# Kernel tuning notes

Hardware: AMD Instinct MI355X
Metric: run time of the kernel (lower is better)

## Reference

```python
import jax, jax.numpy as jnp
import numpy as np

HIDDEN = 128
SIGMA_D = 0.2
SIGMA_A = 15.0
ANGLE_K = 10
FACTOR_A = 180.0 / (SIGMA_A * np.pi)


def _div_term():
    half = HIDDEN // 2
    return jnp.exp(jnp.arange(half, dtype=jnp.float32) * (-np.log(10000.0) / half))


def _sinusoid(x):
    # x: float tensor of (integer-valued) indices; returns x.shape + (HIDDEN,)
    pos = x[..., None].astype(jnp.float32)
    dt = _div_term()
    s = jnp.sin(pos * dt)
    c = jnp.cos(pos * dt)
    # interleave: even channels sin, odd channels cos
    return jnp.stack([s, c], axis=-1).reshape(x.shape + (HIDDEN,))


def setup_inputs() -> dict:
    key = jax.random.key(0)
    k1, k2, k3, k4, k5 = jax.random.split(key, 5)
    B, N = 2, 1024
    scale = 1.0 / np.sqrt(HIDDEN)
    points = jax.random.normal(k1, (B, N, 3), dtype=jnp.float32)
    Wd = jax.random.normal(k2, (HIDDEN, HIDDEN), dtype=jnp.float32) * scale
    bd = jax.random.normal(k3, (HIDDEN,), dtype=jnp.float32) * scale
    Wa = jax.random.normal(k4, (HIDDEN, HIDDEN), dtype=jnp.float32) * scale
    ba = jax.random.normal(k5, (HIDDEN,), dtype=jnp.float32) * scale
    return {"points": points, "Wd": Wd, "bd": bd, "Wa": Wa, "ba": ba}


def _single(pts, Wd, bd, Wa, ba):
    # pts: (N, 3)
    n = pts.shape[0]
    diff = pts[:, None, :] - pts[None, :, :]            # (N, N, 3)
    dists = jnp.sqrt(jnp.sum(diff * diff, axis=-1))      # (N, N)
    idx_d = jnp.clip(jnp.round(dists / SIGMA_D), 0.0, 255.0)
    # k nearest neighbours (smallest distances, incl. self)
    _, nn = jax.lax.top_k(-dists, ANGLE_K)               # (N, K)
    vec = pts[nn] - pts[:, None, :]                      # (N, K, 3)
    vnorm = jnp.linalg.norm(vec, axis=-1, keepdims=True)
    unit = vec / (vnorm + 1e-8)
    cos_ang = jnp.clip(jnp.einsum('nkd,nld->nkl', unit, unit), -1.0, 1.0)
    angles = jnp.arccos(cos_ang)                         # (N, K, K)
    idx_a = jnp.clip(jnp.round(angles * FACTOR_A), 0.0, 255.0)
    # indices computed under no_grad in the original
    idx_d = jax.lax.stop_gradient(idx_d)
    idx_a = jax.lax.stop_gradient(idx_a)

    embed_d = _sinusoid(idx_d)                           # (N, N, C)
    embed_d = jnp.mean(embed_d @ Wd.T + bd, axis=1)      # (N, C)

    embed_a = _sinusoid(idx_a)                           # (N, K, K, C)
    embed_a = embed_a @ Wa.T + ba
    embed_a = jnp.max(embed_a.reshape(n, -1, HIDDEN), axis=1)  # (N, C)
    return embed_d + embed_a


def reference(points, Wd, bd, Wa, ba):
    return jax.vmap(_single, in_axes=(0, None, None, None, None))(points, Wd, bd, Wa, ba)
```

## Files before the change

kernel.cpp:

```cpp
#include <hip/hip_runtime.h>
#include <hip/hip_bf16.h>

#define NPTS 1024
#define HID 128
#define KNN 10
#define PPB 4
#define FLT_MAX_ 3.402823466e+38f

__global__ __launch_bounds__(512) void gse_build(
    const float* __restrict__ Wd, const float* __restrict__ bd,
    const float* __restrict__ Wa, const float* __restrict__ ba,
    const float* __restrict__ pts, int nP,
    float* __restrict__ Td, float* __restrict__ Ta, float4* __restrict__ P4) {
    const int blk = blockIdx.x;
    const int tid = threadIdx.x;

    if (tid < 8) {
        for (int idx = blk * 8 + tid; idx < nP; idx += 272 * 8) {
            P4[idx] = make_float4(pts[idx * 3 + 0], pts[idx * 3 + 1],
                                  pts[idx * 3 + 2], 0.0f);
        }
    }

    __shared__ float S[HID];
    __shared__ float part[512];
    const bool isA = (blk >= 256);
    const int v = isA ? blk - 256 : blk;
    const int c = tid & 127;
    const int seg = tid >> 7;

    if (tid < HID) {
        const int m = tid >> 1;
        const float dtm = expf((float)m * (float)(-9.210340371976184 / 64.0));
        const float arg = (float)v * dtm;
        S[tid] = (tid & 1) ? cosf(arg) : sinf(arg);
    }
    __syncthreads();

    const float* W = isA ? Wa : Wd;
    const float* wrow = W + c * HID + seg * 32;
    const float* srow = S + seg * 32;
    float acc = 0.0f;
    #pragma unroll
    for (int h = 0; h < 32; h += 4) {
        const float4 wv = *reinterpret_cast<const float4*>(wrow + h);
        acc += srow[h] * wv.x + srow[h + 1] * wv.y + srow[h + 2] * wv.z + srow[h + 3] * wv.w;
    }
    part[tid] = acc;
    __syncthreads();

    if (tid < HID) {
        const float s = (part[c] + part[c + 128]) + (part[c + 256] + part[c + 384]);
        if (isA) Ta[v * HID + c] = s + ba[c];
        else     Td[v * HID + c] = (s + bd[c]) * (1.0f / (float)NPTS);
    }
}

__global__ __launch_bounds__(1024, 8) void gse_main4(
    const float4* __restrict__ P4,
    const float* __restrict__ Td,
    const float* __restrict__ Ta,
    float* __restrict__ out) {
    const int tid = threadIdx.x;
    const int pt  = tid >> 8;
    const int t   = tid & 255;
    const int lane = tid & 63;
    const int w   = (tid >> 6) & 3;
    const int gid = blockIdx.x * PPB + pt;

    const int b = gid >> 10;
    const int i = gid & 1023;
    const float4* P = P4 + (size_t)b * NPTS;

    __shared__ int h4[PPB][4][256];
    __shared__ unsigned long long cand[PPB][64];
    __shared__ int nn[PPB][KNN];
    __shared__ float sums[PPB][256], mxs[PPB][256];
    __shared__ unsigned amask_s[PPB];
    __shared__ int ccnt[PPB];
    __shared__ int meta_s[PPB];

    {
        int* hf = (int*)h4[pt];
        hf[t] = 0; hf[t + 256] = 0; hf[t + 512] = 0; hf[t + 768] = 0;
    }
    if (t == 0) { amask_s[pt] = 0u; ccnt[pt] = 0; }
    const float4 p = P[i];
    __syncthreads();

    float d4[4];
    int q4[4];
    const int jb = w * 256;
    #pragma unroll
    for (int s = 0; s < 4; ++s) {
        const int j = jb + s * 64 + lane;
        const float4 q = P[j];
        const float dx = p.x - q.x;
        const float dy = p.y - q.y;
        const float dz = p.z - q.z;
        const float dd = sqrtf(dx * dx + dy * dy + dz * dz);
        d4[s] = dd;
        float qq = rintf(dd / 0.2f);
        qq = fminf(fmaxf(qq, 0.0f), 255.0f);
        q4[s] = (int)qq;
        atomicAdd(&h4[pt][w][q4[s]], 1);
    }
    __syncthreads();

    const int hsum = h4[pt][0][t] + h4[pt][1][t] + h4[pt][2][t] + h4[pt][3][t];
    h4[pt][0][t] = hsum;
    __syncthreads();
    const int* hist = h4[pt][0];

    if (w == 0) {
        int cum = hist[lane];
        #pragma unroll
        for (int off = 1; off < 64; off <<= 1) {
            const int n_ = __shfl_up(cum, off);
            if (lane >= off) cum += n_;
        }
        const unsigned long long bal = __ballot(cum >= KNN);
        const unsigned long long nz0 = __ballot(hist[lane] != 0);
        const unsigned long long nz1 = __ballot(hist[64 + lane] != 0);
        const unsigned long long nz2 = __ballot(hist[128 + lane] != 0);
        const unsigned long long nz3 = __ballot(hist[192 + lane] != 0);
        int maxbin;
        if (nz3)      maxbin = 192 + 63 - __clzll((long long)nz3);
        else if (nz2) maxbin = 128 + 63 - __clzll((long long)nz2);
        else if (nz1) maxbin = 64 + 63 - __clzll((long long)nz1);
        else          maxbin = 63 - __clzll((long long)nz0);
        int b10 = 0, c = 0;
        if (bal) { b10 = __ffsll(bal) - 1; c = __shfl(cum, b10); }
        const int fast = (bal != 0ull && c <= 64) ? 1 : 0;
        if (lane == 0) {
            meta_s[pt] = (b10 & 0xff) | ((fast ? c : 0) << 8)
                       | ((maxbin & 0xff) << 16) | (fast << 30);
        }
    }
    __syncthreads();
    const int meta = meta_s[pt];
    const int b10 = meta & 0xff;
    const int c = (meta >> 8) & 0xff;
    const int maxbin = (meta >> 16) & 0xff;
    const bool fast = ((meta >> 30) & 1) != 0;

    if (fast) {
        #pragma unroll
        for (int s = 0; s < 4; ++s) {
            const bool pred = (q4[s] <= b10);
            const unsigned long long m = __ballot(pred);
            if (m) {
                int base = 0;
                if (lane == 0) base = atomicAdd(&ccnt[pt], __popcll(m));
                base = __shfl(base, 0);
                if (pred) {
                    const int pos = base + (int)__popcll(m & ((1ull << lane) - 1ull));
                    const int idx = jb + s * 64 + lane;
                    cand[pt][pos] = ((unsigned long long)__float_as_uint(d4[s]) << 32)
                                  | (unsigned)idx;
                }
            }
        }
        __syncthreads();
        if (t < c) {
            const unsigned long long my = cand[pt][t];
            int rank = 0;
            #pragma unroll 8
            for (int pp = 0; pp < c; ++pp) {
                rank += (cand[pt][pp] < my) ? 1 : 0;
            }
            if (rank < KNN) nn[pt][rank] = (int)(my & 0xffffffffu);
        }
        __syncthreads();
    } else {
        unsigned valid = 0xfu;
        unsigned long long keep = 0;
        for (int r = 0; r < KNN; ++r) {
            float bv = FLT_MAX_;
            int bi = 0x7fffffff;
            #pragma unroll
            for (int s = 0; s < 4; ++s) {
                if (valid & (1u << s)) {
                    const float v_ = d4[s];
                    const int id_ = jb + s * 64 + lane;
                    if (v_ < bv || (v_ == bv && id_ < bi)) { bv = v_; bi = id_; }
                }
            }
            #pragma unroll
            for (int off = 32; off > 0; off >>= 1) {
                const float ov = __shfl_xor(bv, off);
                const int oi = __shfl_xor(bi, off);
                if (ov < bv || (ov == bv && oi < bi)) { bv = ov; bi = oi; }
            }
            const int loc = bi - jb;
            if (loc >= 0 && loc < 256 && lane == (loc & 63)) valid &= ~(1u << (loc >> 6));
            if (lane == r) keep = ((unsigned long long)__float_as_uint(bv) << 32)
                                | (unsigned)bi;
        }
        if (lane < KNN) cand[pt][w * KNN + lane] = keep;
        __syncthreads();
        if (t < 4 * KNN) {
            const unsigned long long my = cand[pt][t];
            int rank = 0;
            for (int pp = 0; pp < 4 * KNN; ++pp) {
                rank += (cand[pt][pp] < my) ? 1 : 0;
            }
            if (rank < KNN) nn[pt][rank] = (int)(my & 0xffffffffu);
        }
        __syncthreads();
    }

    if (t < KNN * KNN) {
        const int k = t / KNN, l = t % KNN;
        const int jk = nn[pt][k], jl = nn[pt][l];
        const float4 qk = P[jk];
        const float4 ql = P[jl];
        const float kx = qk.x - p.x;
        const float ky = qk.y - p.y;
        const float kz = qk.z - p.z;
        const float dk = sqrtf(kx * kx + ky * ky + kz * kz) + 1e-8f;
        const float lx = ql.x - p.x;
        const float ly = ql.y - p.y;
        const float lz = ql.z - p.z;
        const float dl = sqrtf(lx * lx + ly * ly + lz * lz) + 1e-8f;
        float cc = (kx / dk) * (lx / dl) + (ky / dk) * (ly / dl) + (kz / dk) * (lz / dl);
        cc = fminf(fmaxf(cc, -1.0f), 1.0f);
        const float ang = acosf(cc);
        float q = rintf(ang * (float)(180.0 / (15.0 * M_PI)));
        q = fminf(fmaxf(q, 0.0f), 15.0f);
        atomicOr(&amask_s[pt], 1u << (int)q);
    }
    __syncthreads();

    const unsigned am = amask_s[pt];
    const int c7 = t & 127;
    const int half = t >> 7;
    float s = 0.0f;
    const float* tdc = Td + c7;
    #pragma unroll 4
    for (int v = half; v <= maxbin; v += 2) {
        s += (float)hist[v] * tdc[v * HID];
    }
    float mx = -FLT_MAX_;
    const float* tac = Ta + c7;
    #pragma unroll
    for (int v = 0; v < 8; ++v) {
        const int vv = half * 8 + v;
        const float tv = tac[vv * HID];
        if (am & (1u << vv)) mx = fmaxf(mx, tv);
    }
    sums[pt][t] = s;
    mxs[pt][t] = mx;
    __syncthreads();
    if (t < HID) {
        out[(size_t)gid * HID + t] =
            (sums[pt][t] + sums[pt][t + 128]) + fmaxf(mxs[pt][t], mxs[pt][t + 128]);
    }
}

__global__ __launch_bounds__(256, 8) void gse_main(
    const float4* __restrict__ P4,
    const float* __restrict__ Td,
    const float* __restrict__ Ta,
    float* __restrict__ out) {
    const int gid = blockIdx.x;
    const int b = gid >> 10;
    const int i = gid & 1023;
    const float4* P = P4 + (size_t)b * NPTS;
    const int tid = threadIdx.x;
    const int lane = tid & 63;
    const int w = tid >> 6;

    __shared__ int h4[4][256];
    __shared__ unsigned long long cand[64];
    __shared__ int nn[KNN];
    __shared__ float sums[256], mxs[256];
    __shared__ unsigned amask_s;
    __shared__ int ccnt;
    __shared__ int meta_s;

    {
        int* hf = (int*)h4;
        hf[tid] = 0; hf[tid + 256] = 0; hf[tid + 512] = 0; hf[tid + 768] = 0;
    }
    if (tid == 0) { amask_s = 0u; ccnt = 0; }
    const float4 p = P[i];
    __syncthreads();

    float d4[4];
    int q4[4];
    const int jb = w * 256;
    #pragma unroll
    for (int s = 0; s < 4; ++s) {
        const int j = jb + s * 64 + lane;
        const float4 q = P[j];
        const float dx = p.x - q.x;
        const float dy = p.y - q.y;
        const float dz = p.z - q.z;
        const float dd = sqrtf(dx * dx + dy * dy + dz * dz);
        d4[s] = dd;
        float qq = rintf(dd / 0.2f);
        qq = fminf(fmaxf(qq, 0.0f), 255.0f);
        q4[s] = (int)qq;
        atomicAdd(&h4[w][q4[s]], 1);
    }
    __syncthreads();

    const int hsum = h4[0][tid] + h4[1][tid] + h4[2][tid] + h4[3][tid];
    h4[0][tid] = hsum;
    __syncthreads();
    const int* hist = h4[0];

    if (w == 0) {
        int cum = hist[lane];
        #pragma unroll
        for (int off = 1; off < 64; off <<= 1) {
            const int n_ = __shfl_up(cum, off);
            if (lane >= off) cum += n_;
        }
        const unsigned long long bal = __ballot(cum >= KNN);
        const unsigned long long nz0 = __ballot(hist[lane] != 0);
        const unsigned long long nz1 = __ballot(hist[64 + lane] != 0);
        const unsigned long long nz2 = __ballot(hist[128 + lane] != 0);
        const unsigned long long nz3 = __ballot(hist[192 + lane] != 0);
        int maxbin;
        if (nz3)      maxbin = 192 + 63 - __clzll((long long)nz3);
        else if (nz2) maxbin = 128 + 63 - __clzll((long long)nz2);
        else if (nz1) maxbin = 64 + 63 - __clzll((long long)nz1);
        else          maxbin = 63 - __clzll((long long)nz0);
        int b10 = 0, c = 0;
        if (bal) { b10 = __ffsll(bal) - 1; c = __shfl(cum, b10); }
        const int fast = (bal != 0ull && c <= 64) ? 1 : 0;
        if (lane == 0) {
            meta_s = (b10 & 0xff) | ((fast ? c : 0) << 8)
                   | ((maxbin & 0xff) << 16) | (fast << 30);
        }
    }
    __syncthreads();
    const int meta = meta_s;
    const int b10 = meta & 0xff;
    const int c = (meta >> 8) & 0xff;
    const int maxbin = (meta >> 16) & 0xff;
    const bool fast = ((meta >> 30) & 1) != 0;

    if (fast) {
        #pragma unroll
        for (int s = 0; s < 4; ++s) {
            const bool pred = (q4[s] <= b10);
            const unsigned long long m = __ballot(pred);
            if (m) {
                int base = 0;
                if (lane == 0) base = atomicAdd(&ccnt, __popcll(m));
                base = __shfl(base, 0);
                if (pred) {
                    const int pos = base + (int)__popcll(m & ((1ull << lane) - 1ull));
                    const int idx = jb + s * 64 + lane;
                    cand[pos] = ((unsigned long long)__float_as_uint(d4[s]) << 32)
                              | (unsigned)idx;
                }
            }
        }
        __syncthreads();
        if (tid < c) {
            const unsigned long long my = cand[tid];
            int rank = 0;
            #pragma unroll 8
            for (int pp = 0; pp < c; ++pp) rank += (cand[pp] < my) ? 1 : 0;
            if (rank < KNN) nn[rank] = (int)(my & 0xffffffffu);
        }
        __syncthreads();
    } else {
        unsigned valid = 0xfu;
        unsigned long long keep = 0;
        for (int r = 0; r < KNN; ++r) {
            float bv = FLT_MAX_;
            int bi = 0x7fffffff;
            #pragma unroll
            for (int s = 0; s < 4; ++s) {
                if (valid & (1u << s)) {
                    const float v_ = d4[s];
                    const int id_ = jb + s * 64 + lane;
                    if (v_ < bv || (v_ == bv && id_ < bi)) { bv = v_; bi = id_; }
                }
            }
            #pragma unroll
            for (int off = 32; off > 0; off >>= 1) {
                const float ov = __shfl_xor(bv, off);
                const int oi = __shfl_xor(bi, off);
                if (ov < bv || (ov == bv && oi < bi)) { bv = ov; bi = oi; }
            }
            const int loc = bi - jb;
            if (loc >= 0 && loc < 256 && lane == (loc & 63)) valid &= ~(1u << (loc >> 6));
            if (lane == r) keep = ((unsigned long long)__float_as_uint(bv) << 32)
                                | (unsigned)bi;
        }
        if (lane < KNN) cand[w * KNN + lane] = keep;
        __syncthreads();
        if (tid < 4 * KNN) {
            const unsigned long long my = cand[tid];
            int rank = 0;
            for (int pp = 0; pp < 4 * KNN; ++pp) rank += (cand[pp] < my) ? 1 : 0;
            if (rank < KNN) nn[rank] = (int)(my & 0xffffffffu);
        }
        __syncthreads();
    }

    if (tid < KNN * KNN) {
        const int k = tid / KNN, l = tid % KNN;
        const int jk = nn[k], jl = nn[l];
        const float4 qk = P[jk];
        const float4 ql = P[jl];
        const float kx = qk.x - p.x;
        const float ky = qk.y - p.y;
        const float kz = qk.z - p.z;
        const float dk = sqrtf(kx * kx + ky * ky + kz * kz) + 1e-8f;
        const float lx = ql.x - p.x;
        const float ly = ql.y - p.y;
        const float lz = ql.z - p.z;
        const float dl = sqrtf(lx * lx + ly * ly + lz * lz) + 1e-8f;
        float cc = (kx / dk) * (lx / dl) + (ky / dk) * (ly / dl) + (kz / dk) * (lz / dl);
        cc = fminf(fmaxf(cc, -1.0f), 1.0f);
        const float ang = acosf(cc);
        float q = rintf(ang * (float)(180.0 / (15.0 * M_PI)));
        q = fminf(fmaxf(q, 0.0f), 15.0f);
        atomicOr(&amask_s, 1u << (int)q);
    }
    __syncthreads();

    const unsigned am = amask_s;
    const int c7 = tid & 127;
    const int half = tid >> 7;
    float s = 0.0f;
    const float* tdc = Td + c7;
    #pragma unroll 4
    for (int v = half; v <= maxbin; v += 2) {
        s += (float)hist[v] * tdc[v * HID];
    }
    float mx = -FLT_MAX_;
    const float* tac = Ta + c7;
    #pragma unroll
    for (int v = 0; v < 8; ++v) {
        const int vv = half * 8 + v;
        const float tv = tac[vv * HID];
        if (am & (1u << vv)) mx = fmaxf(mx, tv);
    }
    sums[tid] = s;
    mxs[tid] = mx;
    __syncthreads();
    if (tid < HID) {
        out[(size_t)gid * HID + tid] =
            (sums[tid] + sums[tid + 128]) + fmaxf(mxs[tid], mxs[tid + 128]);
    }
}

extern "C" void kernel_launch(void* const* d_in, const int* in_sizes, int n_in,
                              void* d_out, int out_size, void* d_ws, size_t ws_size,
                              hipStream_t stream) {
    const float* pts = (const float*)d_in[0];
    const float* Wd  = (const float*)d_in[1];
    const float* bd  = (const float*)d_in[2];
    const float* Wa  = (const float*)d_in[3];
    const float* ba  = (const float*)d_in[4];
    float* out = (float*)d_out;

    const int B = in_sizes[0] / (NPTS * 3);
    const int nP = B * NPTS;

    float* Td = (float*)d_ws;
    float* Ta = Td + 256 * HID;
    float4* P4 = (float4*)(Ta + 16 * HID);

    gse_build<<<272, 512, 0, stream>>>(Wd, bd, Wa, ba, pts, nP, Td, Ta, P4);
    if (nP % PPB == 0) {
        gse_main4<<<nP / PPB, PPB * 256, 0, stream>>>(P4, Td, Ta, out);
    } else {
        gse_main<<<nP, 256, 0, stream>>>(P4, Td, Ta, out);
    }
}
```

Before: 21.83 us.

## Specialize wavefronts per point to overlap kNN rank, angle mask and histogram matvec

```diff
diff --git a/kernel.cpp b/kernel.cpp
--- a/kernel.cpp
+++ b/kernel.cpp
@@ -4,7 +4,7 @@
 #define NPTS 1024
 #define HID 128
 #define KNN 10
-#define PPB 4
+#define PPB 2
 #define FLT_MAX_ 3.402823466e+38f
 
 __global__ __launch_bounds__(512) void gse_build(
@@ -16,7 +16,7 @@
     const int tid = threadIdx.x;
 
     if (tid < 8) {
-        for (int idx = blk * 8 + tid; idx < nP; idx += 272 * 8) {
+        for (int idx = blk * 8 + tid; idx < nP; idx += 256 * 8) {
             P4[idx] = make_float4(pts[idx * 3 + 0], pts[idx * 3 + 1],
                                   pts[idx * 3 + 2], 0.0f);
         }
@@ -24,8 +24,7 @@
 
     __shared__ float S[HID];
     __shared__ float part[512];
-    const bool isA = (blk >= 256);
-    const int v = isA ? blk - 256 : blk;
+    const int v = blk;
     const int c = tid & 127;
     const int seg = tid >> 7;
 
@@ -37,26 +36,45 @@
     }
     __syncthreads();
 
-    const float* W = isA ? Wa : Wd;
-    const float* wrow = W + c * HID + seg * 32;
-    const float* srow = S + seg * 32;
-    float acc = 0.0f;
-    #pragma unroll
-    for (int h = 0; h < 32; h += 4) {
-        const float4 wv = *reinterpret_cast<const float4*>(wrow + h);
-        acc += srow[h] * wv.x + srow[h + 1] * wv.y + srow[h + 2] * wv.z + srow[h + 3] * wv.w;
-    }
-    part[tid] = acc;
-    __syncthreads();
-
+    {
+        const float* wrow = Wd + c * HID + seg * 32;
+        const float* srow = S + seg * 32;
+        float acc = 0.0f;
+        #pragma unroll
+        for (int h = 0; h < 32; h += 4) {
+            const float4 wv = *reinterpret_cast<const float4*>(wrow + h);
+            acc += srow[h] * wv.x + srow[h + 1] * wv.y
+                 + srow[h + 2] * wv.z + srow[h + 3] * wv.w;
+        }
+        part[tid] = acc;
+    }
+    __syncthreads();
     if (tid < HID) {
         const float s = (part[c] + part[c + 128]) + (part[c + 256] + part[c + 384]);
-        if (isA) Ta[v * HID + c] = s + ba[c];
-        else     Td[v * HID + c] = (s + bd[c]) * (1.0f / (float)NPTS);
+        Td[v * HID + c] = (s + bd[c]) * (1.0f / (float)NPTS);
+    }
+
+    if (blk < 16) {
+        __syncthreads();
+        const float* wrow = Wa + c * HID + seg * 32;
+        const float* srow = S + seg * 32;
+        float acc = 0.0f;
+        #pragma unroll
+        for (int h = 0; h < 32; h += 4) {
+            const float4 wv = *reinterpret_cast<const float4*>(wrow + h);
+            acc += srow[h] * wv.x + srow[h + 1] * wv.y
+                 + srow[h + 2] * wv.z + srow[h + 3] * wv.w;
+        }
+        part[tid] = acc;
+        __syncthreads();
+        if (tid < HID) {
+            const float s = (part[c] + part[c + 128]) + (part[c + 256] + part[c + 384]);
+            Ta[v * HID + c] = s + ba[c];
+        }
     }
 }
 
-__global__ __launch_bounds__(1024, 8) void gse_main4(
+__global__ __launch_bounds__(512, 8) void gse_main2(
     const float4* __restrict__ P4,
     const float* __restrict__ Td,
     const float* __restrict__ Ta,
@@ -75,7 +93,6 @@
     __shared__ int h4[PPB][4][256];
     __shared__ unsigned long long cand[PPB][64];
     __shared__ int nn[PPB][KNN];
-    __shared__ float sums[PPB][256], mxs[PPB][256];
     __shared__ unsigned amask_s[PPB];
     __shared__ int ccnt[PPB];
     __shared__ int meta_s[PPB];
@@ -84,7 +101,7 @@
         int* hf = (int*)h4[pt];
         hf[t] = 0; hf[t + 256] = 0; hf[t + 512] = 0; hf[t + 768] = 0;
     }
-    if (t == 0) { amask_s[pt] = 0u; ccnt[pt] = 0; }
+    if (t == 0) { ccnt[pt] = 0; }
     const float4 p = P[i];
     __syncthreads();
 
@@ -161,17 +178,6 @@
                 }
             }
         }
-        __syncthreads();
-        if (t < c) {
-            const unsigned long long my = cand[pt][t];
-            int rank = 0;
-            #pragma unroll 8
-            for (int pp = 0; pp < c; ++pp) {
-                rank += (cand[pt][pp] < my) ? 1 : 0;
-            }
-            if (rank < KNN) nn[pt][rank] = (int)(my & 0xffffffffu);
-        }
-        __syncthreads();
     } else {
         unsigned valid = 0xfu;
         unsigned long long keep = 0;
@@ -198,63 +204,81 @@
                                 | (unsigned)bi;
         }
         if (lane < KNN) cand[pt][w * KNN + lane] = keep;
-        __syncthreads();
-        if (t < 4 * KNN) {
-            const unsigned long long my = cand[pt][t];
+    }
+    __syncthreads();
+
+    const int ncand = fast ? c : 4 * KNN;
+    const int vsplit = (maxbin < 15) ? maxbin : 15;
+    float s = 0.0f;
+
+    if (w == 2) {
+        if (lane < ncand) {
+            const unsigned long long my = cand[pt][lane];
             int rank = 0;
-            for (int pp = 0; pp < 4 * KNN; ++pp) {
+            #pragma unroll 8
+            for (int pp = 0; pp < ncand; ++pp) {
                 rank += (cand[pt][pp] < my) ? 1 : 0;
             }
             if (rank < KNN) nn[pt][rank] = (int)(my & 0xffffffffu);
         }
-        __syncthreads();
-    }
-
-    if (t < KNN * KNN) {
-        const int k = t / KNN, l = t % KNN;
-        const int jk = nn[pt][k], jl = nn[pt][l];
-        const float4 qk = P[jk];
-        const float4 ql = P[jl];
-        const float kx = qk.x - p.x;
-        const float ky = qk.y - p.y;
-        const float kz = qk.z - p.z;
-        const float dk = sqrtf(kx * kx + ky * ky + kz * kz) + 1e-8f;
-        const float lx = ql.x - p.x;
-        const float ly = ql.y - p.y;
-        const float lz = ql.z - p.z;
-        const float dl = sqrtf(lx * lx + ly * ly + lz * lz) + 1e-8f;
-        float cc = (kx / dk) * (lx / dl) + (ky / dk) * (ly / dl) + (kz / dk) * (lz / dl);
-        cc = fminf(fmaxf(cc, -1.0f), 1.0f);
-        const float ang = acosf(cc);
-        float q = rintf(ang * (float)(180.0 / (15.0 * M_PI)));
-        q = fminf(fmaxf(q, 0.0f), 15.0f);
-        atomicOr(&amask_s[pt], 1u << (int)q);
-    }
-    __syncthreads();
-
-    const unsigned am = amask_s[pt];
-    const int c7 = t & 127;
-    const int half = t >> 7;
-    float s = 0.0f;
-    const float* tdc = Td + c7;
-    #pragma unroll 4
-    for (int v = half; v <= maxbin; v += 2) {
-        s += (float)hist[v] * tdc[v * HID];
-    }
-    float mx = -FLT_MAX_;
-    const float* tac = Ta + c7;
-    #pragma unroll
-    for (int v = 0; v < 8; ++v) {
-        const int vv = half * 8 + v;
-        const float tv = tac[vv * HID];
-        if (am & (1u << vv)) mx = fmaxf(mx, tv);
-    }
-    sums[pt][t] = s;
-    mxs[pt][t] = mx;
-    __syncthreads();
+    } else if (w < 2) {
+        const float* tdc = Td + t;
+        #pragma unroll 4
+        for (int v = 0; v <= vsplit; ++v) {
+            s += (float)hist[v] * tdc[v * HID];
+        }
+    }
+    __syncthreads();
+
+    if (w == 3) {
+        unsigned mk = 0u;
+        #pragma unroll
+        for (int rep = 0; rep < 2; ++rep) {
+            const int pr = lane + rep * 64;
+            const int valid_p = (pr < KNN * KNN);
+            const int k = valid_p ? (pr / KNN) : 0;
+            const int l = valid_p ? (pr % KNN) : 0;
+            const int jk = nn[pt][k], jl = nn[pt][l];
+            const float4 qk = P[jk];
+            const float4 ql = P[jl];
+            const float kx = qk.x - p.x;
+            const float ky = qk.y - p.y;
+            const float kz = qk.z - p.z;
+            const float dk = sqrtf(kx * kx + ky * ky + kz * kz) + 1e-8f;
+            const float lx = ql.x - p.x;
+            const float ly = ql.y - p.y;
+            const float lz = ql.z - p.z;
+            const float dl = sqrtf(lx * lx + ly * ly + lz * lz) + 1e-8f;
+            float cc = (kx / dk) * (lx / dl) + (ky / dk) * (ly / dl)
+                     + (kz / dk) * (lz / dl);
+            cc = fminf(fmaxf(cc, -1.0f), 1.0f);
+            const float ang = acosf(cc);
+            float q = rintf(ang * (float)(180.0 / (15.0 * M_PI)));
+            q = fminf(fmaxf(q, 0.0f), 15.0f);
+            if (valid_p) mk |= 1u << (int)q;
+        }
+        #pragma unroll
+        for (int off = 32; off > 0; off >>= 1) mk |= __shfl_xor(mk, off);
+        if (lane == 0) amask_s[pt] = mk;
+    } else if (w < 2) {
+        const float* tdc = Td + t;
+        #pragma unroll 4
+        for (int v = 16; v <= maxbin; ++v) {
+            s += (float)hist[v] * tdc[v * HID];
+        }
+    }
+    __syncthreads();
+
     if (t < HID) {
-        out[(size_t)gid * HID + t] =
-            (sums[pt][t] + sums[pt][t + 128]) + fmaxf(mxs[pt][t], mxs[pt][t + 128]);
+        const unsigned am = amask_s[pt];
+        float mx = -FLT_MAX_;
+        const float* tac = Ta + t;
+        #pragma unroll
+        for (int v = 0; v < 16; ++v) {
+            const float tv = tac[v * HID];
+            if (am & (1u << v)) mx = fmaxf(mx, tv);
+        }
+        out[(size_t)gid * HID + t] = s + mx;
     }
 }
 
@@ -470,9 +494,9 @@
     float* Ta = Td + 256 * HID;
     float4* P4 = (float4*)(Ta + 16 * HID);
 
-    gse_build<<<272, 512, 0, stream>>>(Wd, bd, Wa, ba, pts, nP, Td, Ta, P4);
+    gse_build<<<256, 512, 0, stream>>>(Wd, bd, Wa, ba, pts, nP, Td, Ta, P4);
     if (nP % PPB == 0) {
-        gse_main4<<<nP / PPB, PPB * 256, 0, stream>>>(P4, Td, Ta, out);
+        gse_main2<<<nP / PPB, PPB * 256, 0, stream>>>(P4, Td, Ta, out);
     } else {
         gse_main<<<nP, 256, 0, stream>>>(P4, Td, Ta, out);
     }
```

After: 21.10 us. -3.3%, faster.

## Halve points per block and cut barriers in histogram and KNN phases

Applied to the files above, without the earlier changes.

```diff
diff --git a/kernel.cpp b/kernel.cpp
--- a/kernel.cpp
+++ b/kernel.cpp
@@ -4,7 +4,7 @@
 #define NPTS 1024
 #define HID 128
 #define KNN 10
-#define PPB 4
+#define PPB 2
 #define FLT_MAX_ 3.402823466e+38f
 
 __global__ __launch_bounds__(512) void gse_build(
@@ -56,7 +56,7 @@
     }
 }
 
-__global__ __launch_bounds__(1024, 8) void gse_main4(
+__global__ __launch_bounds__(512, 8) void gse_main2(
     const float4* __restrict__ P4,
     const float* __restrict__ Td,
     const float* __restrict__ Ta,
@@ -73,6 +73,7 @@
     const float4* P = P4 + (size_t)b * NPTS;
 
     __shared__ int h4[PPB][4][256];
+    __shared__ int hm[PPB][256];
     __shared__ unsigned long long cand[PPB][64];
     __shared__ int nn[PPB][KNN];
     __shared__ float sums[PPB][256], mxs[PPB][256];
@@ -80,13 +81,10 @@
     __shared__ int ccnt[PPB];
     __shared__ int meta_s[PPB];
 
-    {
-        int* hf = (int*)h4[pt];
-        hf[t] = 0; hf[t + 256] = 0; hf[t + 512] = 0; hf[t + 768] = 0;
-    }
+    #pragma unroll
+    for (int k = 0; k < 4; ++k) h4[pt][w][lane + k * 64] = 0;
     if (t == 0) { amask_s[pt] = 0u; ccnt[pt] = 0; }
     const float4 p = P[i];
-    __syncthreads();
 
     float d4[4];
     int q4[4];
@@ -107,23 +105,26 @@
     }
     __syncthreads();
 
-    const int hsum = h4[pt][0][t] + h4[pt][1][t] + h4[pt][2][t] + h4[pt][3][t];
-    h4[pt][0][t] = hsum;
-    __syncthreads();
-    const int* hist = h4[pt][0];
-
     if (w == 0) {
-        int cum = hist[lane];
+        const int* H0 = h4[pt][0];
+        const int* H1 = h4[pt][1];
+        const int* H2 = h4[pt][2];
+        const int* H3 = h4[pt][3];
+        const int hv0 = H0[lane] + H1[lane] + H2[lane] + H3[lane];
+        int cum = hv0;
         #pragma unroll
         for (int off = 1; off < 64; off <<= 1) {
             const int n_ = __shfl_up(cum, off);
             if (lane >= off) cum += n_;
         }
         const unsigned long long bal = __ballot(cum >= KNN);
-        const unsigned long long nz0 = __ballot(hist[lane] != 0);
-        const unsigned long long nz1 = __ballot(hist[64 + lane] != 0);
-        const unsigned long long nz2 = __ballot(hist[128 + lane] != 0);
-        const unsigned long long nz3 = __ballot(hist[192 + lane] != 0);
+        const int hv1 = H0[64 + lane] + H1[64 + lane] + H2[64 + lane] + H3[64 + lane];
+        const int hv2 = H0[128 + lane] + H1[128 + lane] + H2[128 + lane] + H3[128 + lane];
+        const int hv3 = H0[192 + lane] + H1[192 + lane] + H2[192 + lane] + H3[192 + lane];
+        const unsigned long long nz0 = __ballot(hv0 != 0);
+        const unsigned long long nz1 = __ballot(hv1 != 0);
+        const unsigned long long nz2 = __ballot(hv2 != 0);
+        const unsigned long long nz3 = __ballot(hv3 != 0);
         int maxbin;
         if (nz3)      maxbin = 192 + 63 - __clzll((long long)nz3);
         else if (nz2) maxbin = 128 + 63 - __clzll((long long)nz2);
@@ -135,6 +136,18 @@
         if (lane == 0) {
             meta_s[pt] = (b10 & 0xff) | ((fast ? c : 0) << 8)
                        | ((maxbin & 0xff) << 16) | (fast << 30);
+        }
+    } else if (w == 1) {
+        #pragma unroll
+        for (int k = 0; k < 2; ++k) {
+            const int v = lane + k * 64;
+            hm[pt][v] = h4[pt][0][v] + h4[pt][1][v] + h4[pt][2][v] + h4[pt][3][v];
+        }
+    } else if (w == 2) {
+        #pragma unroll
+        for (int k = 2; k < 4; ++k) {
+            const int v = lane + k * 64;
+            hm[pt][v] = h4[pt][0][v] + h4[pt][1][v] + h4[pt][2][v] + h4[pt][3][v];
         }
     }
     __syncthreads();
@@ -161,17 +174,6 @@
                 }
             }
         }
-        __syncthreads();
-        if (t < c) {
-            const unsigned long long my = cand[pt][t];
-            int rank = 0;
-            #pragma unroll 8
-            for (int pp = 0; pp < c; ++pp) {
-                rank += (cand[pt][pp] < my) ? 1 : 0;
-            }
-            if (rank < KNN) nn[pt][rank] = (int)(my & 0xffffffffu);
-        }
-        __syncthreads();
     } else {
         unsigned valid = 0xfu;
         unsigned long long keep = 0;
@@ -198,17 +200,20 @@
                                 | (unsigned)bi;
         }
         if (lane < KNN) cand[pt][w * KNN + lane] = keep;
-        __syncthreads();
-        if (t < 4 * KNN) {
-            const unsigned long long my = cand[pt][t];
-            int rank = 0;
-            for (int pp = 0; pp < 4 * KNN; ++pp) {
-                rank += (cand[pt][pp] < my) ? 1 : 0;
-            }
-            if (rank < KNN) nn[pt][rank] = (int)(my & 0xffffffffu);
-        }
-        __syncthreads();
-    }
+    }
+    __syncthreads();
+
+    const int ncand = fast ? c : 4 * KNN;
+    if (t < ncand) {
+        const unsigned long long my = cand[pt][t];
+        int rank = 0;
+        #pragma unroll 8
+        for (int pp = 0; pp < ncand; ++pp) {
+            rank += (cand[pt][pp] < my) ? 1 : 0;
+        }
+        if (rank < KNN) nn[pt][rank] = (int)(my & 0xffffffffu);
+    }
+    __syncthreads();
 
     if (t < KNN * KNN) {
         const int k = t / KNN, l = t % KNN;
@@ -239,7 +244,7 @@
     const float* tdc = Td + c7;
     #pragma unroll 4
     for (int v = half; v <= maxbin; v += 2) {
-        s += (float)hist[v] * tdc[v * HID];
+        s += (float)hm[pt][v] * tdc[v * HID];
     }
     float mx = -FLT_MAX_;
     const float* tac = Ta + c7;
@@ -472,7 +477,7 @@
 
     gse_build<<<272, 512, 0, stream>>>(Wd, bd, Wa, ba, pts, nP, Td, Ta, P4);
     if (nP % PPB == 0) {
-        gse_main4<<<nP / PPB, PPB * 256, 0, stream>>>(P4, Td, Ta, out);
+        gse_main2<<<nP / PPB, PPB * 256, 0, stream>>>(P4, Td, Ta, out);
     } else {
         gse_main<<<nP, 256, 0, stream>>>(P4, Td, Ta, out);
     }
```

New measurement: 20.38 us. -6.6%, faster.
